# Kernel optimization log

Hardware: AMD Instinct MI355X
Metric: run time of the kernel (lower is better)

The kernel has to match this reference:

```python
import jax, jax.numpy as jnp
import numpy as np

IN_CHANNELS = 64
OUT_CHANNELS = 64
SEQ_LEN = 512
KERNEL_SIZE = 9
STRIDE = 1
PADDING = 4  # symmetric
OUT_SEQ_LEN = (SEQ_LEN + 2 * PADDING - (KERNEL_SIZE - 1) - 1) // STRIDE + 1  # 512


def setup_inputs() -> dict:
    key = jax.random.key(0)
    k1, k2, k3 = jax.random.split(key, 3)
    x = jax.random.normal(k1, (64, IN_CHANNELS, SEQ_LEN), dtype=jnp.float32)
    # nn.init.normal_(std=0.1)
    weight = 0.1 * jax.random.normal(k2, (IN_CHANNELS, OUT_CHANNELS, KERNEL_SIZE, OUT_SEQ_LEN), dtype=jnp.float32)
    bias = 0.1 * jax.random.normal(k3, (OUT_CHANNELS, OUT_SEQ_LEN), dtype=jnp.float32)
    return {"x": x, "weight": weight, "bias": bias}


def reference(x, weight, bias):
    # x: [B, Ci, S] -> pad last dim
    xp = jnp.pad(x, ((0, 0), (0, 0), (PADDING, PADDING)))
    # Unfold (im2col) as a gather: same math as the one-hot grouped conv.
    starts = jnp.arange(OUT_SEQ_LEN) * STRIDE            # [L]
    offs = jnp.arange(KERNEL_SIZE)                        # [K]
    idx = starts[:, None] + offs[None, :]                 # [L, K]
    patches = xp[:, :, idx]                               # [B, Ci, L, K]
    # per-position matmul: 'b i l k, i o k l -> b o l'
    out = jnp.einsum('bilk,iokl->bol', patches, weight)
    out = out + bias                                      # [B, Co, L]
    return out
```

## Files before the change

### kernel.cpp

```cpp
#include <hip/hip_runtime.h>


#define CIN   64
#define COUT  64
#define SEQ   512
#define KS    9
#define LT    16
#define OT    8
#define LWIN  24
#define WSTR  (COUT*KS*SEQ)
#define XBS   40
#define XLW   (64*XBS)
#define XS_ELEMS (LWIN*XLW)
#define BOS   40
#define BLS   328
#define BSLOT (LT*BLS)
#define ZOFF  (XS_ELEMS + 2*BSLOT)
#define LDS_USH (ZOFF + 64)
#define LDS_BYTES (LDS_USH*2)
#define NSTEP 18

typedef __attribute__((ext_vector_type(8))) short bf16x8;
typedef __attribute__((ext_vector_type(4))) float f32x4;

__device__ __forceinline__ uint pack2bf(float a0, float a1) {
    uint u0 = __float_as_uint(a0) + 0x8000u;
    uint u1 = __float_as_uint(a1) + 0x8000u;
    return __builtin_amdgcn_perm(u1, u0, 0x07060302);
}

#define BAR() do {                                                           \
    asm volatile("s_waitcnt lgkmcnt(0)" ::: "memory");                       \
    __builtin_amdgcn_s_barrier();                                            \
    asm volatile("" ::: "memory");                                           \
} while (0)

#define WAITV(n) do {                                                        \
    asm volatile("s_waitcnt vmcnt(" #n ")" ::: "memory");                    \
    __builtin_amdgcn_sched_barrier(0);                                       \
} while (0)

__global__ __launch_bounds__(1024, 4)
void lc1d_mfma(const float* __restrict__ x, const float* __restrict__ w,
               const float* __restrict__ bias, float* __restrict__ out)
{
    extern __shared__ ushort lds[];
    ushort* Xs = lds;
    ushort* BsB = lds + XS_ELEMS;

    const int tid  = threadIdx.x;
    const int lane = tid & 63;
    const int wvid = tid >> 6;
    const int bt = wvid & 3;
    const int lg = wvid >> 2;
    const int lt = blockIdx.x >> 3;
    const int os = blockIdx.x & 7;
    const int l0 = lt * LT;
    const int o0 = os * OT;

    const bool stager = (tid < 512);
    const int lf  = tid & 3;
    const int oo  = (tid >> 2) & 7;
    const int ipp = (tid >> 5) & 15;

    const float* wbase = w + ((size_t)(2*ipp)*COUT + (o0 + oo))*(KS*SEQ) + l0 + lf*4;

    f32x4 rA[3], rB[3];

    #define LOAD_RING(sl, s) if (stager && (s) < NSTEP) {                        \
        const int ih_ = (s) / 9, k_ = (s) - 9*((s)/9);                           \
        const float* pA_ = wbase + (size_t)ih_*32*WSTR + k_*SEQ;                 \
        const float* pB_ = pA_ + WSTR;                                           \
        asm volatile("global_load_dwordx4 %0, %1, off"                           \
                     : "=&v"(rA[sl]) : "v"(pA_));                                \
        asm volatile("global_load_dwordx4 %0, %1, off"                           \
                     : "=&v"(rB[sl]) : "v"(pB_));                                \
    }

    #define WRITE_BS(sl, s) {                                                    \
        ushort* dst_ = BsB + ((s)&1)*BSLOT + oo*BOS + 2*ipp;                     \
        _Pragma("unroll")                                                        \
        for (int dl = 0; dl < 4; ++dl) {                                         \
            uint pk_ = pack2bf(rA[sl][dl], rB[sl][dl]);                          \
            *(uint*)(dst_ + (lf*4+dl)*BLS) = pk_;                                \
        }                                                                        \
    }

    #define STAGE_XS(ih) {                                                       \
        const int qq  = tid & 7;                                                 \
        const int rp0 = tid >> 3;                                                \
        const int cr_ = (qq & 3) << 3;                                           \
        if (qq < 6) {                                                            \
            _Pragma("unroll")                                                    \
            for (int it = 0; it < 8; ++it) {                                     \
                const int rp = rp0 + it*128;                                     \
                const int b_ = rp >> 4, ip_ = rp & 15;                           \
                const float* s0 = x + ((size_t)(b_*CIN) + (ih)*32 + 2*ip_)*SEQ   \
                                    + (l0 - 4) + qq*4;                           \
                float4 v0 = make_float4(0.f,0.f,0.f,0.f), v1 = v0;               \
                if (!((lt == 0 && qq == 0) || (lt == 31 && qq == 5))) {          \
                    v0 = *(const float4*)s0;                                     \
                    v1 = *(const float4*)(s0 + SEQ);                             \
                }                                                                \
                ushort* d_ = Xs + b_*XBS + ((2*ip_ + cr_) & 31);                 \
                _Pragma("unroll")                                                \
                for (int dl = 0; dl < 4; ++dl)                                   \
                    *(uint*)(d_ + (qq*4+dl)*XLW) = pack2bf((&v0.x)[dl],          \
                                                           (&v1.x)[dl]);         \
            }                                                                    \
        }                                                                        \
    }

    const int abase = (bt*16 + (lane & 15))*XBS;
    const int ks_   = lane >> 4;
    const int boff  = (lane & 15)*BOS + ks_*8;
    const bool nhi  = (lane & 15) >= 8;
    const ushort* zptr = lds + ZOFF + ks_*8;

    f32x4 acc[4];
    #pragma unroll
    for (int j = 0; j < 4; ++j) acc[j] = (f32x4)0.0f;

    #define DO_MFMA(s) {                                                         \
        const int k_ = (s) % 9;                                                  \
        const ushort* BsS = BsB + ((s)&1)*BSLOT;                                 \
        bf16x8 Af[4], Bf[4];                                                     \
        _Pragma("unroll")                                                        \
        for (int dl = 0; dl < 4; ++dl) {                                         \
            const int ll  = lg*4 + dl;                                           \
            const int row = ll + k_;                                             \
            const int col = ((ks_ + (row >> 2)) & 3) << 3;                       \
            Af[dl] = *(const bf16x8*)(Xs + row*XLW + abase + col);               \
            Bf[dl] = *(const bf16x8*)(nhi ? zptr : (BsS + ll*BLS + boff));       \
        }                                                                        \
        _Pragma("unroll")                                                        \
        for (int dl = 0; dl < 4; ++dl)                                           \
            acc[dl] = __builtin_amdgcn_mfma_f32_16x16x32_bf16(Af[dl], Bf[dl],    \
                                                              acc[dl], 0, 0, 0); \
    }

    #define STEP(s, wv) {                                                        \
        if (stager && (s) < NSTEP-1) {                                           \
            WAITV(wv);                                                           \
            WRITE_BS(((s)+1)%3, (s)+1)                                           \
        }                                                                        \
        LOAD_RING(((s)+1)%3, (s)+4)                                              \
        DO_MFMA(s)                                                               \
        BAR();                                                                   \
    }

    LOAD_RING(0, 0)
    LOAD_RING(1, 1)
    LOAD_RING(2, 2)
    if (tid < 64) lds[ZOFF + tid] = 0;
    STAGE_XS(0)
    if (stager) {
        WAITV(0);
        WRITE_BS(0, 0)
    }
    LOAD_RING(0, 3)
    BAR();

    STEP(0,4)  STEP(1,4)  STEP(2,4)  STEP(3,4)  STEP(4,4)
    STEP(5,4)  STEP(6,4)  STEP(7,4)  STEP(8,4)

    STAGE_XS(1)
    BAR();

    STEP(9,4)   STEP(10,4) STEP(11,4) STEP(12,4) STEP(13,4)
    STEP(14,4)  STEP(15,2) STEP(16,0) STEP(17,0)

    if (!nhi) {
        const int og = o0 + (lane & 15);
        const int rb = ks_*4;
        #pragma unroll
        for (int dl = 0; dl < 4; ++dl) {
            const int lgl = l0 + lg*4 + dl;
            const float bv = bias[og*SEQ + lgl];
            #pragma unroll
            for (int r = 0; r < 4; ++r) {
                const int bg = bt*16 + rb + r;
                out[((size_t)(bg*COUT + og))*SEQ + lgl] = acc[dl][r] + bv;
            }
        }
    }
}

extern "C" void kernel_launch(void* const* d_in, const int* in_sizes, int n_in,
                              void* d_out, int out_size, void* d_ws, size_t ws_size,
                              hipStream_t stream) {
    const float* x    = (const float*)d_in[0];
    const float* wgt  = (const float*)d_in[1];
    const float* bias = (const float*)d_in[2];
    float* out        = (float*)d_out;

    hipFuncSetAttribute((const void*)lc1d_mfma,
                        hipFuncAttributeMaxDynamicSharedMemorySize, LDS_BYTES);
    dim3 grid(256);
    lc1d_mfma<<<grid, 1024, LDS_BYTES, stream>>>(x, wgt, bias, out);
}
```

Measured before the change: 133.6 us.

## Split batch across four smaller blocks to raise grid parallelism

The work is re-partitioned so that each block covers 16 batch rows instead of all 64. Blocks shrink from 1024 to 256 threads and the grid grows from 256 to 1024, with all threads now staging weights (four loads per step instead of two). The aim is to improve latency hiding and occupancy, with several smaller blocks per CU overlapping their load and compute phases. In exchange, each weight tile is fetched by four blocks instead of one, which multiplies weight traffic unless L2 or MALL absorbs the repeats.

```diff
diff --git a/kernel.cpp b/kernel.cpp
--- a/kernel.cpp
+++ b/kernel.cpp
@@ -8,9 +8,10 @@
 #define LT    16
 #define OT    8
 #define LWIN  24
+#define BB    16
 #define WSTR  (COUT*KS*SEQ)
-#define XBS   40
-#define XLW   (64*XBS)
+#define XBS   36
+#define XLW   (BB*XBS)
 #define XS_ELEMS (LWIN*XLW)
 #define BOS   40
 #define BLS   328
@@ -40,7 +41,7 @@
     __builtin_amdgcn_sched_barrier(0);                                       \
 } while (0)
 
-__global__ __launch_bounds__(1024, 4)
+__global__ __launch_bounds__(256, 3)
 void lc1d_mfma(const float* __restrict__ x, const float* __restrict__ w,
                const float* __restrict__ bias, float* __restrict__ out)
 {
@@ -50,39 +51,47 @@
 
     const int tid  = threadIdx.x;
     const int lane = tid & 63;
-    const int wvid = tid >> 6;
-    const int bt = wvid & 3;
-    const int lg = wvid >> 2;
-    const int lt = blockIdx.x >> 3;
+    const int lg   = tid >> 6;
+    const int lt = blockIdx.x >> 5;
+    const int q  = (blockIdx.x >> 3) & 3;
     const int os = blockIdx.x & 7;
     const int l0 = lt * LT;
     const int o0 = os * OT;
-
-    const bool stager = (tid < 512);
+    const int b0 = q * BB;
+
     const int lf  = tid & 3;
     const int oo  = (tid >> 2) & 7;
-    const int ipp = (tid >> 5) & 15;
+    const int ipp = (tid >> 5) & 7;
 
     const float* wbase = w + ((size_t)(2*ipp)*COUT + (o0 + oo))*(KS*SEQ) + l0 + lf*4;
 
-    f32x4 rA[3], rB[3];
-
-    #define LOAD_RING(sl, s) if (stager && (s) < NSTEP) {                        \
+    f32x4 rA[3][2], rB[3][2];
+
+    #define LOAD_RING(sl, s) if ((s) < NSTEP) {                                  \
         const int ih_ = (s) / 9, k_ = (s) - 9*((s)/9);                           \
-        const float* pA_ = wbase + (size_t)ih_*32*WSTR + k_*SEQ;                 \
-        const float* pB_ = pA_ + WSTR;                                           \
-        asm volatile("global_load_dwordx4 %0, %1, off"                           \
-                     : "=&v"(rA[sl]) : "v"(pA_));                                \
-        asm volatile("global_load_dwordx4 %0, %1, off"                           \
-                     : "=&v"(rB[sl]) : "v"(pB_));                                \
+        const float* p0_ = wbase + (size_t)ih_*32*WSTR + k_*SEQ;                 \
+        const float* p1_ = p0_ + WSTR;                                           \
+        const float* p2_ = p0_ + 16*WSTR;                                        \
+        const float* p3_ = p0_ + 17*WSTR;                                        \
+        asm volatile("global_load_dwordx4 %0, %1, off"                           \
+                     : "=&v"(rA[sl][0]) : "v"(p0_));                             \
+        asm volatile("global_load_dwordx4 %0, %1, off"                           \
+                     : "=&v"(rB[sl][0]) : "v"(p1_));                             \
+        asm volatile("global_load_dwordx4 %0, %1, off"                           \
+                     : "=&v"(rA[sl][1]) : "v"(p2_));                             \
+        asm volatile("global_load_dwordx4 %0, %1, off"                           \
+                     : "=&v"(rB[sl][1]) : "v"(p3_));                             \
     }
 
     #define WRITE_BS(sl, s) {                                                    \
         ushort* dst_ = BsB + ((s)&1)*BSLOT + oo*BOS + 2*ipp;                     \
         _Pragma("unroll")                                                        \
-        for (int dl = 0; dl < 4; ++dl) {                                         \
-            uint pk_ = pack2bf(rA[sl][dl], rB[sl][dl]);                          \
-            *(uint*)(dst_ + (lf*4+dl)*BLS) = pk_;                                \
+        for (int g = 0; g < 2; ++g) {                                            \
+            _Pragma("unroll")                                                    \
+            for (int dl = 0; dl < 4; ++dl) {                                     \
+                uint pk_ = pack2bf(rA[sl][g][dl], rB[sl][g][dl]);                \
+                *(uint*)(dst_ + g*16 + (lf*4+dl)*BLS) = pk_;                     \
+            }                                                                    \
         }                                                                        \
     }
 
@@ -93,10 +102,10 @@
         if (qq < 6) {                                                            \
             _Pragma("unroll")                                                    \
             for (int it = 0; it < 8; ++it) {                                     \
-                const int rp = rp0 + it*128;                                     \
+                const int rp = rp0 + it*32;                                      \
                 const int b_ = rp >> 4, ip_ = rp & 15;                           \
-                const float* s0 = x + ((size_t)(b_*CIN) + (ih)*32 + 2*ip_)*SEQ   \
-                                    + (l0 - 4) + qq*4;                           \
+                const float* s0 = x + ((size_t)((b0 + b_)*CIN) + (ih)*32         \
+                                       + 2*ip_)*SEQ + (l0 - 4) + qq*4;           \
                 float4 v0 = make_float4(0.f,0.f,0.f,0.f), v1 = v0;               \
                 if (!((lt == 0 && qq == 0) || (lt == 31 && qq == 5))) {          \
                     v0 = *(const float4*)s0;                                     \
@@ -111,7 +120,7 @@
         }                                                                        \
     }
 
-    const int abase = (bt*16 + (lane & 15))*XBS;
+    const int abase = (lane & 15)*XBS;
     const int ks_   = lane >> 4;
     const int boff  = (lane & 15)*BOS + ks_*8;
     const bool nhi  = (lane & 15) >= 8;
@@ -140,7 +149,7 @@
     }
 
     #define STEP(s, wv) {                                                        \
-        if (stager && (s) < NSTEP-1) {                                           \
+        if ((s) < NSTEP-1) {                                                     \
             WAITV(wv);                                                           \
             WRITE_BS(((s)+1)%3, (s)+1)                                           \
         }                                                                        \
@@ -154,21 +163,19 @@
     LOAD_RING(2, 2)
     if (tid < 64) lds[ZOFF + tid] = 0;
     STAGE_XS(0)
-    if (stager) {
-        WAITV(0);
-        WRITE_BS(0, 0)
-    }
+    WAITV(0);
+    WRITE_BS(0, 0)
     LOAD_RING(0, 3)
     BAR();
 
-    STEP(0,4)  STEP(1,4)  STEP(2,4)  STEP(3,4)  STEP(4,4)
-    STEP(5,4)  STEP(6,4)  STEP(7,4)  STEP(8,4)
+    STEP(0,8)  STEP(1,8)  STEP(2,8)  STEP(3,8)  STEP(4,8)
+    STEP(5,8)  STEP(6,8)  STEP(7,8)  STEP(8,8)
 
     STAGE_XS(1)
     BAR();
 
-    STEP(9,4)   STEP(10,4) STEP(11,4) STEP(12,4) STEP(13,4)
-    STEP(14,4)  STEP(15,2) STEP(16,0) STEP(17,0)
+    STEP(9,8)   STEP(10,8) STEP(11,8) STEP(12,8) STEP(13,8)
+    STEP(14,8)  STEP(15,4) STEP(16,0) STEP(17,0)
 
     if (!nhi) {
         const int og = o0 + (lane & 15);
@@ -179,7 +186,7 @@
             const float bv = bias[og*SEQ + lgl];
             #pragma unroll
             for (int r = 0; r < 4; ++r) {
-                const int bg = bt*16 + rb + r;
+                const int bg = b0 + rb + r;
                 out[((size_t)(bg*COUT + og))*SEQ + lgl] = acc[dl][r] + bv;
             }
         }
@@ -196,6 +203,6 @@
 
     hipFuncSetAttribute((const void*)lc1d_mfma,
                         hipFuncAttributeMaxDynamicSharedMemorySize, LDS_BYTES);
-    dim3 grid(256);
-    lc1d_mfma<<<grid, 1024, LDS_BYTES, stream>>>(x, wgt, bias, out);
+    dim3 grid(1024);
+    lc1d_mfma<<<grid, 256, LDS_BYTES, stream>>>(x, wgt, bias, out);
 }
```

After: 160.8 us. 1.2x slower.
